# Performance work log

Measured on AMD Instinct MI355X. Metric: run time of the kernel, lower is better.

## Reference

```python
import jax, jax.numpy as jnp
import numpy as np
import math

H = 8        # num_heads
D = 1024     # per-head dim (d_q = d_k = d_v)
D_I = 1024   # image embed dim
D_L = 768    # sentence embed dim
EPS = 1e-5   # nn.LayerNorm default


def setup_inputs() -> dict:
    key = jax.random.key(0)
    ks = jax.random.split(key, 8)
    B, NQ, NK = 8, 196, 128
    img_embed = jax.random.normal(ks[0], (B, NQ, D_I), dtype=jnp.float32)
    sent_embed = jax.random.normal(ks[1], (B, NK, D_L), dtype=jnp.float32)
    atten_mask = jnp.ones((B, NK), dtype=jnp.int32)
    # weights stored [in, out] (equivalent to torch Linear weight.T), no bias
    Wq = jax.random.normal(ks[2], (D_I, H * D), dtype=jnp.float32) * (1.0 / math.sqrt(D_I))
    Wk = jax.random.normal(ks[3], (D_L, H * D), dtype=jnp.float32) * (1.0 / math.sqrt(D_L))
    Wv = jax.random.normal(ks[4], (D_L, H * D), dtype=jnp.float32) * (1.0 / math.sqrt(D_L))
    Wo = jax.random.normal(ks[5], (H * D, D_I), dtype=jnp.float32) * (1.0 / math.sqrt(H * D))
    gamma = jnp.ones((D_I,), dtype=jnp.float32)
    beta = jnp.zeros((D_I,), dtype=jnp.float32)
    return {"img_embed": img_embed, "sent_embed": sent_embed, "atten_mask": atten_mask,
            "Wq": Wq, "Wk": Wk, "Wv": Wv, "Wo": Wo, "gamma": gamma, "beta": beta}


def reference(img_embed, sent_embed, atten_mask, Wq, Wk, Wv, Wo, gamma, beta):
    B = img_embed.shape[0]
    # projections -> [B, N, H, D] -> [B, H, N, D]
    Q = (img_embed @ Wq).reshape(B, -1, H, D).transpose(0, 2, 1, 3)
    K = (sent_embed @ Wk).reshape(B, -1, H, D).transpose(0, 2, 1, 3)
    V = (sent_embed @ Wv).reshape(B, -1, H, D).transpose(0, 2, 1, 3)
    # scaled dot-product scores [B, H, NQ, NK]
    score = jnp.einsum('bhqd,bhkd->bhqk', Q, K) / math.sqrt(D)
    mask = (atten_mask != 0)[:, None, None, :]  # [B,1,1,NK]
    score = jnp.where(mask, score, -jnp.inf)
    attn = jax.nn.softmax(score, axis=-1)
    # PV -> [B, NQ, H, D] -> [B, NQ, H*D]
    ctx = jnp.einsum('bhqk,bhkd->bqhd', attn, V).reshape(B, -1, H * D)
    out = ctx @ Wo + img_embed  # residual
    # LayerNorm over last dim
    mu = jnp.mean(out, axis=-1, keepdims=True)
    var = jnp.var(out, axis=-1, keepdims=True)
    return (out - mu) * jax.lax.rsqrt(var + EPS) * gamma + beta
```

## Files before the change

kernel.cpp:

```cpp
#include <hip/hip_runtime.h>
#include <hip/hip_bf16.h>

#define BB 8
#define NQ 196
#define NKK 128
#define HH 8
#define DH 1024
#define DI 1024
#define DL 768
#define HD 8192
#define KSPLIT 8
#define MTOT (BB * NQ)
#define CHK (MTOT * DH)
#define KVCHK (1024 * 1024)

typedef __attribute__((ext_vector_type(8))) short short8;
typedef __attribute__((ext_vector_type(4))) float f32x4;

__device__ inline unsigned short f2bf(float f) {
  unsigned int x = __float_as_uint(f);
  unsigned int r = (x + 0x7fffu + ((x >> 16) & 1u)) >> 16;
  return (unsigned short)r;
}

__device__ inline void gload16(const unsigned short* g, unsigned short* l) {
  __builtin_amdgcn_global_load_lds(
      (const __attribute__((address_space(1))) void*)g,
      (__attribute__((address_space(3))) void*)l, 16, 0, 0);
}

__device__ __attribute__((always_inline)) inline unsigned ldsOff(const unsigned short* p) {
  return (unsigned)(unsigned long long)
      (__attribute__((address_space(3))) const unsigned short*)p;
}

__device__ __attribute__((always_inline)) inline void gload16a(
    const unsigned short* g, unsigned m0off) {
  unsigned s = __builtin_amdgcn_readfirstlane(m0off);
  asm volatile("s_mov_b32 m0, %1\n\t"
               "global_load_lds_dwordx4 %0, off"
               :: "v"(g), "s"(s) : "m0");
}

__global__ __launch_bounds__(256) void k_prep(
    const float* __restrict__ Wq, const float* __restrict__ Wk,
    const float* __restrict__ Wv, const float* __restrict__ Wo,
    const float* __restrict__ img, const float* __restrict__ sent,
    unsigned short* __restrict__ WqT, unsigned short* __restrict__ WkvT,
    unsigned short* __restrict__ WoT,
    unsigned short* __restrict__ imgB, unsigned short* __restrict__ sentB) {
  int b = blockIdx.x, t = threadIdx.x;
  if (b >= 7168) {
    const float* in; unsigned short* out; int i;
    if (b < 7952) { in = img;  out = imgB;  i = ((b - 7168) * 256 + t) * 8; }
    else          { in = sent; out = sentB; i = ((b - 7952) * 256 + t) * 8; }
    float4 x = *reinterpret_cast<const float4*>(in + i);
    float4 y = *reinterpret_cast<const float4*>(in + i + 4);
    short8 v;
    v[0] = (short)f2bf(x.x); v[1] = (short)f2bf(x.y);
    v[2] = (short)f2bf(x.z); v[3] = (short)f2bf(x.w);
    v[4] = (short)f2bf(y.x); v[5] = (short)f2bf(y.y);
    v[6] = (short)f2bf(y.z); v[7] = (short)f2bf(y.w);
    *reinterpret_cast<short8*>(out + i) = v;
    return;
  }
  const float* in; unsigned short* out; int R, C, bx; bool kcb = false;
  if (b < 2048)      { in = Wq; out = WqT;  R = DI; C = HD; bx = b; }
  else if (b < 3584) { in = Wk; out = WkvT; R = DL; C = HD; bx = b - 2048; }
  else if (b < 5120) { in = Wv; out = WkvT + (size_t)HD * DL; R = DL; C = HD; bx = b - 3584; }
  else               { in = Wo; out = WoT;  R = HD; C = DI; bx = b - 5120; kcb = true; }
  int nxc = C >> 6;
  int c0 = (bx % nxc) << 6, r0 = (bx / nxc) << 6;
  __shared__ float tile[64][65];
#pragma unroll
  for (int p = 0; p < 4; ++p) {
    int row = p * 16 + (t >> 4), c4 = (t & 15) << 2;
    float4 v = *reinterpret_cast<const float4*>(&in[(size_t)(r0 + row) * C + c0 + c4]);
    tile[row][c4] = v.x; tile[row][c4 + 1] = v.y;
    tile[row][c4 + 2] = v.z; tile[row][c4 + 3] = v.w;
  }
  __syncthreads();
#pragma unroll
  for (int p = 0; p < 2; ++p) {
    int cc = p * 32 + (t >> 3), r8 = (t & 7) << 3;
    short8 w;
#pragma unroll
    for (int j = 0; j < 8; ++j) w[j] = (short)f2bf(tile[r8 + j][cc]);
    size_t off;
    if (kcb)
      off = ((size_t)(r0 >> 10) << 20) + (size_t)(c0 + cc) * 1024 + (r0 & 1023) + r8;
    else
      off = (size_t)(c0 + cc) * R + r0 + r8;
    *reinterpret_cast<short8*>(&out[off]) = w;
  }
}

__global__ __launch_bounds__(256) void k_transpose_v(
    const unsigned short* __restrict__ Vbase, unsigned short* __restrict__ Vt) {
  __shared__ unsigned short tile[32][34];
  int z = blockIdx.z, b = z >> 3, h = z & 7;
  const unsigned short* in = Vbase + ((size_t)h << 20) + (size_t)b * NKK * 1024;
  unsigned short* out = Vt + (size_t)z * DH * NKK;
  int d0 = blockIdx.x * 32, k0 = blockIdx.y * 32;
  {
    int rr = threadIdx.x >> 3, c4 = (threadIdx.x & 7) << 2;
    ushort4 v = *reinterpret_cast<const ushort4*>(&in[(size_t)(k0 + rr) * 1024 + d0 + c4]);
    tile[rr][c4] = v.x; tile[rr][c4 + 1] = v.y;
    tile[rr][c4 + 2] = v.z; tile[rr][c4 + 3] = v.w;
  }
  __syncthreads();
  {
    int cc = threadIdx.x >> 3, r4 = (threadIdx.x & 7) << 2;
    ushort4 w;
    w.x = tile[r4][cc];     w.y = tile[r4 + 1][cc];
    w.z = tile[r4 + 2][cc]; w.w = tile[r4 + 3][cc];
    *reinterpret_cast<ushort4*>(&out[(size_t)(d0 + cc) * NKK + k0 + r4]) = w;
  }
}


__device__ __attribute__((always_inline)) inline void ph_pre() {
  __builtin_amdgcn_s_barrier();
  asm volatile("s_waitcnt lgkmcnt(0)" ::: "memory");
  __builtin_amdgcn_sched_barrier(0);
  __builtin_amdgcn_s_setprio(1);
}
__device__ __attribute__((always_inline)) inline void ph_post() {
  __builtin_amdgcn_s_setprio(0);
  __builtin_amdgcn_s_barrier();
}
__device__ __attribute__((always_inline)) inline void ph_post_vm4() {
  __builtin_amdgcn_s_setprio(0);
  asm volatile("s_waitcnt vmcnt(4)" ::: "memory");
  __builtin_amdgcn_s_barrier();
}
__device__ __attribute__((always_inline)) inline void ph_post_vm0() {
  __builtin_amdgcn_s_setprio(0);
  asm volatile("s_waitcnt vmcnt(0)" ::: "memory");
  __builtin_amdgcn_s_barrier();
}

#define LDA8(d, buf, s)                                                          \
  { _Pragma("unroll") for (int mi = 0; mi < 4; ++mi) {                           \
      const int row_ = wm * 128 + (s) * 64 + mi * 16 + fr;                       \
      d[mi][0] = *reinterpret_cast<const short8*>(&As[buf][row_ * 64 + swz0]);   \
      d[mi][1] = *reinterpret_cast<const short8*>(&As[buf][row_ * 64 + swz1]);   \
    } }
#define LDB8(d, buf, s)                                                          \
  { _Pragma("unroll") for (int ni = 0; ni < 2; ++ni) {                           \
      const int row_ = wn * 64 + (s) * 32 + ni * 16 + fr;                        \
      d[ni][0] = *reinterpret_cast<const short8*>(&Bs[buf][row_ * 64 + swz0]);   \
      d[ni][1] = *reinterpret_cast<const short8*>(&Bs[buf][row_ * 64 + swz1]);   \
    } }
#define MMQ(a, sa, b, sb)                                                        \
  { _Pragma("unroll") for (int kk = 0; kk < 2; ++kk) {                           \
      _Pragma("unroll") for (int mi = 0; mi < 4; ++mi) {                         \
        _Pragma("unroll") for (int ni = 0; ni < 2; ++ni)                         \
          acc[(sa) * 4 + mi][(sb) * 2 + ni] =                                    \
              __builtin_amdgcn_mfma_f32_16x16x32_bf16(                           \
                  a[mi][kk], b[ni][kk], acc[(sa) * 4 + mi][(sb) * 2 + ni], 0, 0, 0); \
      } } }
#define STA8(buf, h, kof)                                                        \
  { gload16a(aS[h][0] + (kof), aL + (buf) * 32768 + (h) * 16384);                \
    gload16a(aS[h][1] + (kof), aL + (buf) * 32768 + (h) * 16384 + 8192); }
#define STB8(buf, h, kof)                                                        \
  { gload16a(bS[h][0] + (kof), bL + (buf) * 32768 + (h) * 16384);                \
    gload16a(bS[h][1] + (kof), bL + (buf) * 32768 + (h) * 16384 + 8192); }

struct GCfg {
  const unsigned short* A; const unsigned short* B; void* C;
  int M, K, lda, ldb, ldc, nx, ny;
  long aKC, bKC, cKC;
};

template<bool C_BF16, bool HB>
__global__ __launch_bounds__(512, 2) void k_gemm8(GCfg c0, GCfg c1, int split) {
  __shared__ unsigned short As[2][16384];
  __shared__ unsigned short Bs[2][16384];

  const int seg = (int)blockIdx.x >= split;
  const GCfg cfg = seg ? c1 : c0;
  const int o = (int)blockIdx.x - (seg ? split : 0);
  const int nseg = seg ? ((int)gridDim.x - split) : split;
  const int qq = nseg >> 3;
  const int g = (o & 7) * qq + (o >> 3);
  const int ybl = g % cfg.ny; int t1 = g / cfg.ny;
  const int xbl = t1 % cfg.nx; const int kc = t1 / cfg.nx;

  const int M = cfg.M, lda = cfg.lda, ldb = cfg.ldb;
  const unsigned short* Ab = cfg.A + (size_t)kc * cfg.aKC;
  const unsigned short* Bb = cfg.B + (size_t)kc * cfg.bKC;

  const int tid = threadIdx.x, lane = tid & 63, wid = tid >> 6;
  const int wm = wid >> 2, wn = wid & 3;
  const int m_base = ybl * 256, n_base = xbl * 256;
  const int fr = lane & 15, qk = lane >> 4;
  const int swz0 = ((qk ^ (fr & 7)) << 3);
  const int swz1 = (((4 + qk) ^ (fr & 7)) << 3);

  const int srow = lane >> 3;
  const int sc8 = (((lane & 7) ^ srow) << 3);
  const unsigned short* aS[2][2];
  const unsigned short* bS[2][2];
#pragma unroll
  for (int h = 0; h < 2; ++h)
#pragma unroll
    for (int j = 0; j < 2; ++j) {
      int rm = m_base + h * 128 + j * 64 + wid * 8 + srow;
      rm = rm < M ? rm : M - 1;
      aS[h][j] = Ab + (size_t)rm * lda + sc8;
      bS[h][j] = Bb + (size_t)(n_base + h * 128 + j * 64 + wid * 8 + srow) * ldb + sc8;
    }
  const unsigned aL = ldsOff(&As[0][0]) + (unsigned)(wid * 1024);
  const unsigned bL = ldsOff(&Bs[0][0]) + (unsigned)(wid * 1024);

  short8 a0[4][2], a1[4][2], b0[2][2], b1[2][2];
  f32x4 acc[8][4] = {};

  const int NT = cfg.K >> 6;
  const int NIT = NT >> 1;

  STB8(0, 0, 0) STB8(0, 1, 0) STA8(0, 0, 0) STA8(0, 1, 0)
  STB8(1, 0, 64) STB8(1, 1, 64)
  asm volatile("s_waitcnt vmcnt(4)" ::: "memory");
  __builtin_amdgcn_s_barrier();

  for (int it = 0; it < NIT - 1; ++it) {
    const int t1k = (2 * it + 1) << 6;
    const int t2k = (2 * it + 2) << 6;
    const int t3k = (2 * it + 3) << 6;
    LDA8(a0, 0, 0) LDB8(b0, 0, 0) STA8(1, 0, t1k)
    ph_pre(); MMQ(a0, 0, b0, 0) ph_post();
    LDB8(b1, 0, 1) STA8(1, 1, t1k)
    ph_pre(); MMQ(a0, 0, b1, 1) ph_post();
    LDA8(a1, 0, 1) STB8(0, 0, t2k)
    ph_pre(); MMQ(a1, 1, b1, 1) ph_post();
    STB8(0, 1, t2k)
    ph_pre(); MMQ(a1, 1, b0, 0) ph_post_vm4();
    LDA8(a0, 1, 0) LDB8(b0, 1, 0) STA8(0, 0, t2k)
    ph_pre(); MMQ(a0, 0, b0, 0) ph_post();
    LDB8(b1, 1, 1) STA8(0, 1, t2k)
    ph_pre(); MMQ(a0, 0, b1, 1) ph_post();
    LDA8(a1, 1, 1) STB8(1, 0, t3k)
    ph_pre(); MMQ(a1, 1, b1, 1) ph_post();
    STB8(1, 1, t3k)
    ph_pre(); MMQ(a1, 1, b0, 0) ph_post_vm4();
  }

  {
    const int tlk = (NT - 1) << 6;
    LDA8(a0, 0, 0) LDB8(b0, 0, 0) STA8(1, 0, tlk)
    ph_pre(); MMQ(a0, 0, b0, 0) ph_post();
    LDB8(b1, 0, 1) STA8(1, 1, tlk)
    ph_pre(); MMQ(a0, 0, b1, 1) ph_post();
    LDA8(a1, 0, 1)
    ph_pre(); MMQ(a1, 1, b1, 1) ph_post();
    ph_pre(); MMQ(a1, 1, b0, 0) ph_post_vm0();
    LDA8(a0, 1, 0) LDB8(b0, 1, 0)
    ph_pre(); MMQ(a0, 0, b0, 0) ph_post();
    LDB8(b1, 1, 1)
    ph_pre(); MMQ(a0, 0, b1, 1) ph_post();
    LDA8(a1, 1, 1)
    ph_pre(); MMQ(a1, 1, b1, 1) ph_post();
    ph_pre(); MMQ(a1, 1, b0, 0)
    __builtin_amdgcn_s_setprio(0);
  }

  const size_t cOff = (size_t)kc * cfg.cKC;
  const int ldc = cfg.ldc;
  const int rq4 = qk * 4;
#pragma unroll
  for (int mi = 0; mi < 8; ++mi) {
#pragma unroll
    for (int ni = 0; ni < 4; ++ni) {
      int col = n_base + wn * 64 + ni * 16 + fr;
#pragma unroll
      for (int i = 0; i < 4; ++i) {
        int row = m_base + wm * 128 + mi * 16 + rq4 + i;
        if (row < M) {
          float val = acc[mi][ni][i];
          size_t off;
          if constexpr (HB)
            off = (size_t)(col >> 10) * cfg.cKC + (size_t)row * ldc + (col & 1023);
          else
            off = cOff + (size_t)row * ldc + col;
          if constexpr (C_BF16) ((unsigned short*)cfg.C)[off] = f2bf(val);
          else                  ((float*)cfg.C)[off] = val;
        }
      }
    }
  }
}

template<bool C_BF16>
__global__ __launch_bounds__(256, 2) void k_gemm3(
    const unsigned short* __restrict__ A, const unsigned short* __restrict__ B,
    void* __restrict__ Cptr,
    int M, int K, int lda, int ldb, int ldc,
    int nx, int ny, int ZBH,
    long aSB, long aSH, long bSB, long bSH, long cSB, long cSH,
    long aKC, long bKC, long cKC) {
  __shared__ unsigned short As[8192];
  __shared__ unsigned short Bs[8192];

  const int nblk = gridDim.x;
  const int qq = nblk >> 3, rr = nblk & 7;
  int g;
  { const int o = blockIdx.x, xcd = o & 7, i = o >> 3;
    g = (xcd < rr ? xcd * (qq + 1) : rr * (qq + 1) + (xcd - rr) * qq) + i; }
  const int ybl = g % ny; int t1 = g / ny;
  const int xbl = t1 % nx; const int zz = t1 / nx;
  const int kc = zz / ZBH, bh = zz % ZBH;
  const int zb = bh >> 3, zh = bh & 7;

  const unsigned short* Ab = A + (size_t)zb * aSB + (size_t)zh * aSH + (size_t)kc * aKC;
  const unsigned short* Bb = B + (size_t)zb * bSB + (size_t)zh * bSH + (size_t)kc * bKC;

  const int tid = threadIdx.x, lane = tid & 63, wid = tid >> 6;
  const int wm = wid >> 1, wn = wid & 1;
  const int m_base = ybl * 128, n_base = xbl * 128;

  const int r0 = wid * 32 + (lane >> 3);
  const int sc8 = (((lane & 7) ^ (lane >> 3)) << 3);
  const unsigned short* aSrc[4];
  const unsigned short* bSrc[4];
#pragma unroll
  for (int p = 0; p < 4; ++p) {
    int rm = m_base + r0 + p * 8; rm = rm < M ? rm : M - 1;
    aSrc[p] = Ab + (size_t)rm * lda + sc8;
    bSrc[p] = Bb + (size_t)(n_base + r0 + p * 8) * ldb + sc8;
  }

  const int fr = lane & 15;
  const int qk = lane >> 4;
  f32x4 acc[4][4] = {};

  for (int k0 = 0; k0 < K; k0 += 64) {
#pragma unroll
    for (int p = 0; p < 4; ++p) gload16(aSrc[p] + k0, &As[wid * 2048 + p * 512]);
#pragma unroll
    for (int p = 0; p < 4; ++p) gload16(bSrc[p] + k0, &Bs[wid * 2048 + p * 512]);
    __syncthreads();
#pragma unroll
    for (int kk = 0; kk < 2; ++kk) {
      short8 af[4], bfr[4];
#pragma unroll
      for (int mi = 0; mi < 4; ++mi) {
        int row = wm * 64 + mi * 16 + fr;
        int swz = ((kk * 4 + qk) ^ (row & 7)) << 3;
        af[mi] = *reinterpret_cast<const short8*>(&As[row * 64 + swz]);
      }
#pragma unroll
      for (int ni = 0; ni < 4; ++ni) {
        int row = wn * 64 + ni * 16 + fr;
        int swz = ((kk * 4 + qk) ^ (row & 7)) << 3;
        bfr[ni] = *reinterpret_cast<const short8*>(&Bs[row * 64 + swz]);
      }
#pragma unroll
      for (int mi = 0; mi < 4; ++mi)
#pragma unroll
        for (int ni = 0; ni < 4; ++ni)
          acc[mi][ni] = __builtin_amdgcn_mfma_f32_16x16x32_bf16(af[mi], bfr[ni], acc[mi][ni], 0, 0, 0);
    }
    __syncthreads();
  }

  const size_t cOff = (size_t)zb * cSB + (size_t)zh * cSH + (size_t)kc * cKC;
  const int rq = qk * 4;
#pragma unroll
  for (int mi = 0; mi < 4; ++mi) {
#pragma unroll
    for (int ni = 0; ni < 4; ++ni) {
      int col = n_base + wn * 64 + ni * 16 + fr;
#pragma unroll
      for (int i = 0; i < 4; ++i) {
        int row = m_base + wm * 64 + mi * 16 + rq + i;
        if (row < M) {
          float val = acc[mi][ni][i];
          size_t off = cOff + (size_t)row * ldc + col;
          if constexpr (C_BF16) ((unsigned short*)Cptr)[off] = f2bf(val);
          else                  ((float*)Cptr)[off] = val;
        }
      }
    }
  }
}

#define S_PART ((size_t)64 * NQ * NKK)
__global__ __launch_bounds__(256) void k_softmax(
    const float* __restrict__ S, unsigned short* __restrict__ P, const int* __restrict__ mask) {
  int row = blockIdx.x * 4 + (threadIdx.x >> 6);
  if (row >= BB * HH * NQ) return;
  int lane = threadIdx.x & 63;
  int b = row / (HH * NQ);
  const float* s = S + (size_t)row * NKK;
  float s0 = (s[lane]      + s[lane + S_PART])      * 0.03125f;
  float s1 = (s[lane + 64] + s[lane + 64 + S_PART]) * 0.03125f;
  const int* mrow = mask + b * NKK;
  if (mrow[lane] == 0)      s0 = -1e30f;
  if (mrow[lane + 64] == 0) s1 = -1e30f;
  float mx = fmaxf(s0, s1);
#pragma unroll
  for (int d = 32; d; d >>= 1) mx = fmaxf(mx, __shfl_xor(mx, d));
  float e0 = __expf(s0 - mx), e1 = __expf(s1 - mx);
  float sum = e0 + e1;
#pragma unroll
  for (int d = 32; d; d >>= 1) sum += __shfl_xor(sum, d);
  float inv = 1.0f / sum;
  P[(size_t)row * NKK + lane]      = f2bf(e0 * inv);
  P[(size_t)row * NKK + lane + 64] = f2bf(e1 * inv);
}

__global__ __launch_bounds__(256) void k_layernorm_red(
    const unsigned short* __restrict__ Parts, const float* __restrict__ resid,
    const float* __restrict__ gamma, const float* __restrict__ beta,
    float* __restrict__ out, int M) {
  int row = blockIdx.x;
  int tid = threadIdx.x;
  const size_t stride = (size_t)M * DI;
  const unsigned short* p = Parts + (size_t)row * DI;
  const float* r = resid + (size_t)row * DI;
  float v[4], sum = 0.f, sq = 0.f;
#pragma unroll
  for (int i = 0; i < 4; ++i) {
    int c = tid + i * 256;
    float acc = r[c];
#pragma unroll
    for (int k = 0; k < KSPLIT; ++k)
      acc += __uint_as_float((unsigned)p[k * stride + c] << 16);
    v[i] = acc; sum += acc; sq += acc * acc;
  }
#pragma unroll
  for (int d = 32; d; d >>= 1) { sum += __shfl_xor(sum, d); sq += __shfl_xor(sq, d); }
  __shared__ float ssum[4], ssq[4];
  int w = tid >> 6;
  if ((tid & 63) == 0) { ssum[w] = sum; ssq[w] = sq; }
  __syncthreads();
  sum = ssum[0] + ssum[1] + ssum[2] + ssum[3];
  sq  = ssq[0]  + ssq[1]  + ssq[2]  + ssq[3];
  float mean = sum * (1.0f / DI);
  float var  = sq * (1.0f / DI) - mean * mean;
  float rstd = rsqrtf(var + 1e-5f);
  float* o = out + (size_t)row * DI;
#pragma unroll
  for (int i = 0; i < 4; ++i) {
    int c = tid + i * 256;
    o[c] = (v[i] - mean) * rstd * gamma[c] + beta[c];
  }
}

extern "C" void kernel_launch(void* const* d_in, const int* in_sizes, int n_in,
                              void* d_out, int out_size, void* d_ws, size_t ws_size,
                              hipStream_t stream) {
  const float* img   = (const float*)d_in[0];
  const float* sent  = (const float*)d_in[1];
  const int*   mask  = (const int*)d_in[2];
  const float* Wq    = (const float*)d_in[3];
  const float* Wk    = (const float*)d_in[4];
  const float* Wv    = (const float*)d_in[5];
  const float* Wo    = (const float*)d_in[6];
  const float* gamma = (const float*)d_in[7];
  const float* beta  = (const float*)d_in[8];
  float* out = (float*)d_out;

  char* ws = (char*)d_ws;
  unsigned short* WoT   = (unsigned short*)(ws);
  unsigned short* WkvT  = (unsigned short*)(ws + 16777216);
  unsigned short* Vt    = (unsigned short*)(ws + 16777216);
  unsigned short* Oac   = (unsigned short*)(ws + 16777216);
  float*          S2    = (float*)         (ws + 33554432);
  unsigned short* P     = (unsigned short*)(ws + 46399488);
  unsigned short* Qb    = (unsigned short*)(ws + 49610752);
  unsigned short* KVb   = (unsigned short*)(ws + 75300864);
  unsigned short* ctx   = (unsigned short*)(ws + 75300864);
  unsigned short* WqT   = (unsigned short*)(ws + 75300864);
  unsigned short* imgB  = (unsigned short*)(ws + 92078080);
  unsigned short* sentB = (unsigned short*)(ws + 108855296);

  dim3 tb(256);
  dim3 tb8(512);

  k_prep<<<dim3(8336), tb, 0, stream>>>(Wq, Wk, Wv, Wo, img, sent,
                                        WqT, WkvT, WoT, imgB, sentB);

  GCfg cfgQ  = { imgB,  WqT,  Qb,  MTOT,     DI, DI, DI, 1024, 32, 7, 0, 0, (long)CHK };
  GCfg cfgKV = { sentB, WkvT, KVb, BB * NKK, DL, DL, DL, 1024, 64, 4, 0, 0, (long)KVCHK };
  k_gemm8<true, true><<<dim3(224 + 256), tb8, 0, stream>>>(cfgQ, cfgKV, 224);

  k_transpose_v<<<dim3(DH / 32, NKK / 32, BB * HH), tb, 0, stream>>>(
      KVb + ((size_t)8 << 20), Vt);

  k_gemm3<false><<<dim3(2 * 1 * 128), tb, 0, stream>>>(
      Qb, KVb, S2, NQ, DH / 2, 1024, 1024, NKK,
      1, 2, 64,
      (long)NQ * 1024, (long)CHK,
      (long)NKK * 1024, (long)KVCHK,
      (long)HH * NQ * NKK, (long)NQ * NKK,
      (long)(DH / 2), (long)(DH / 2), (long)64 * NQ * NKK);

  k_softmax<<<dim3(BB * HH * NQ / 4), tb, 0, stream>>>(S2, P, mask);

  k_gemm3<true><<<dim3(2 * 8 * 64), tb, 0, stream>>>(
      P, Vt, ctx, NQ, NKK, NKK, NKK, 1024,
      8, 2, 64,
      (long)HH * NQ * NKK, (long)NQ * NKK,
      (long)HH * DH * NKK, (long)DH * NKK,
      (long)NQ * 1024, (long)CHK,
      0, 0, 0);

  GCfg cfgO = { ctx, WoT, Oac, MTOT, HD / KSPLIT, 1024, 1024, DI, 4, 7,
                (long)CHK, (long)KVCHK, (long)CHK };
  k_gemm8<true, false><<<dim3(224), tb8, 0, stream>>>(cfgO, cfgO, 224);

  k_layernorm_red<<<dim3(BB * NQ), tb, 0, stream>>>(Oac, img, gamma, beta, out, BB * NQ);
}
```

Before: 177.8 us.

## Merge V transpose into softmax launch and run PV with large-tile GEMM

The standalone V-transpose kernel is folded into the softmax kernel as extra blocks (k_mid), which removes one launch and lets the two independent jobs overlap. The P·V product moves from the small k_gemm3 kernel to the 512-thread k_gemm8 kernel. A new PVF epilogue maps each (batch, head) K-chunk index to the ctx layout, and the grid is 256 blocks covering 4 column tiles by 1 row tile per (b,h). The larger 256-row tile covers only 196 valid rows, so some MFMA work is wasted on padding. Mixing two block types in one grid may also unbalance the schedule.

```diff
diff --git a/kernel.cpp b/kernel.cpp
--- a/kernel.cpp
+++ b/kernel.cpp
@@ -92,29 +92,6 @@
     else
       off = (size_t)(c0 + cc) * R + r0 + r8;
     *reinterpret_cast<short8*>(&out[off]) = w;
-  }
-}
-
-__global__ __launch_bounds__(256) void k_transpose_v(
-    const unsigned short* __restrict__ Vbase, unsigned short* __restrict__ Vt) {
-  __shared__ unsigned short tile[32][34];
-  int z = blockIdx.z, b = z >> 3, h = z & 7;
-  const unsigned short* in = Vbase + ((size_t)h << 20) + (size_t)b * NKK * 1024;
-  unsigned short* out = Vt + (size_t)z * DH * NKK;
-  int d0 = blockIdx.x * 32, k0 = blockIdx.y * 32;
-  {
-    int rr = threadIdx.x >> 3, c4 = (threadIdx.x & 7) << 2;
-    ushort4 v = *reinterpret_cast<const ushort4*>(&in[(size_t)(k0 + rr) * 1024 + d0 + c4]);
-    tile[rr][c4] = v.x; tile[rr][c4 + 1] = v.y;
-    tile[rr][c4 + 2] = v.z; tile[rr][c4 + 3] = v.w;
-  }
-  __syncthreads();
-  {
-    int cc = threadIdx.x >> 3, r4 = (threadIdx.x & 7) << 2;
-    ushort4 w;
-    w.x = tile[r4][cc];     w.y = tile[r4 + 1][cc];
-    w.z = tile[r4 + 2][cc]; w.w = tile[r4 + 3][cc];
-    *reinterpret_cast<ushort4*>(&out[(size_t)(d0 + cc) * NKK + k0 + r4]) = w;
   }
 }
 
@@ -173,7 +150,7 @@
   long aKC, bKC, cKC;
 };
 
-template<bool C_BF16, bool HB>
+template<bool C_BF16, bool HB, bool PVF>
 __global__ __launch_bounds__(512, 2) void k_gemm8(GCfg c0, GCfg c1, int split) {
   __shared__ unsigned short As[2][16384];
   __shared__ unsigned short Bs[2][16384];
@@ -280,7 +257,10 @@
         if (row < M) {
           float val = acc[mi][ni][i];
           size_t off;
-          if constexpr (HB)
+          if constexpr (PVF)
+            off = (size_t)(kc & 7) * cfg.cKC
+                + ((size_t)(kc >> 3) * NQ + row) * 1024 + col;
+          else if constexpr (HB)
             off = (size_t)(col >> 10) * cfg.cKC + (size_t)row * ldc + (col & 1023);
           else
             off = cOff + (size_t)row * ldc + col;
@@ -387,9 +367,34 @@
 }
 
 #define S_PART ((size_t)64 * NQ * NKK)
-__global__ __launch_bounds__(256) void k_softmax(
-    const float* __restrict__ S, unsigned short* __restrict__ P, const int* __restrict__ mask) {
-  int row = blockIdx.x * 4 + (threadIdx.x >> 6);
+__global__ __launch_bounds__(256) void k_mid(
+    const unsigned short* __restrict__ Vbase, unsigned short* __restrict__ Vt,
+    const float* __restrict__ S, unsigned short* __restrict__ P,
+    const int* __restrict__ mask) {
+  __shared__ unsigned short tile[32][34];
+  int blk = blockIdx.x;
+  if (blk < 8192) {
+    int z = blk >> 7, b = z >> 3, h = z & 7;
+    int d0 = (blk & 31) * 32, k0 = ((blk >> 5) & 3) * 32;
+    const unsigned short* in = Vbase + ((size_t)h << 20) + (size_t)b * NKK * 1024;
+    unsigned short* out = Vt + (size_t)z * DH * NKK;
+    {
+      int rr = threadIdx.x >> 3, c4 = (threadIdx.x & 7) << 2;
+      ushort4 v = *reinterpret_cast<const ushort4*>(&in[(size_t)(k0 + rr) * 1024 + d0 + c4]);
+      tile[rr][c4] = v.x; tile[rr][c4 + 1] = v.y;
+      tile[rr][c4 + 2] = v.z; tile[rr][c4 + 3] = v.w;
+    }
+    __syncthreads();
+    {
+      int cc = threadIdx.x >> 3, r4 = (threadIdx.x & 7) << 2;
+      ushort4 w;
+      w.x = tile[r4][cc];     w.y = tile[r4 + 1][cc];
+      w.z = tile[r4 + 2][cc]; w.w = tile[r4 + 3][cc];
+      *reinterpret_cast<ushort4*>(&out[(size_t)(d0 + cc) * NKK + k0 + r4]) = w;
+    }
+    return;
+  }
+  int row = (blk - 8192) * 4 + (threadIdx.x >> 6);
   if (row >= BB * HH * NQ) return;
   int lane = threadIdx.x & 63;
   int b = row / (HH * NQ);
@@ -485,10 +490,7 @@
 
   GCfg cfgQ  = { imgB,  WqT,  Qb,  MTOT,     DI, DI, DI, 1024, 32, 7, 0, 0, (long)CHK };
   GCfg cfgKV = { sentB, WkvT, KVb, BB * NKK, DL, DL, DL, 1024, 64, 4, 0, 0, (long)KVCHK };
-  k_gemm8<true, true><<<dim3(224 + 256), tb8, 0, stream>>>(cfgQ, cfgKV, 224);
-
-  k_transpose_v<<<dim3(DH / 32, NKK / 32, BB * HH), tb, 0, stream>>>(
-      KVb + ((size_t)8 << 20), Vt);
+  k_gemm8<true, true, false><<<dim3(224 + 256), tb8, 0, stream>>>(cfgQ, cfgKV, 224);
 
   k_gemm3<false><<<dim3(2 * 1 * 128), tb, 0, stream>>>(
       Qb, KVb, S2, NQ, DH / 2, 1024, 1024, NKK,
@@ -498,19 +500,16 @@
       (long)HH * NQ * NKK, (long)NQ * NKK,
       (long)(DH / 2), (long)(DH / 2), (long)64 * NQ * NKK);
 
-  k_softmax<<<dim3(BB * HH * NQ / 4), tb, 0, stream>>>(S2, P, mask);
-
-  k_gemm3<true><<<dim3(2 * 8 * 64), tb, 0, stream>>>(
-      P, Vt, ctx, NQ, NKK, NKK, NKK, 1024,
-      8, 2, 64,
-      (long)HH * NQ * NKK, (long)NQ * NKK,
-      (long)HH * DH * NKK, (long)DH * NKK,
-      (long)NQ * 1024, (long)CHK,
-      0, 0, 0);
+  k_mid<<<dim3(8192 + (BB * HH * NQ) / 4), tb, 0, stream>>>(
+      KVb + ((size_t)8 << 20), Vt, S2, P, mask);
+
+  GCfg cfgPV = { P, Vt, ctx, NQ, NKK, NKK, NKK, 1024, 4, 1,
+                 (long)NQ * NKK, (long)DH * NKK, (long)CHK };
+  k_gemm8<true, false, true><<<dim3(256), tb8, 0, stream>>>(cfgPV, cfgPV, 256);
 
   GCfg cfgO = { ctx, WoT, Oac, MTOT, HD / KSPLIT, 1024, 1024, DI, 4, 7,
                 (long)CHK, (long)KVCHK, (long)CHK };
-  k_gemm8<true, false><<<dim3(224), tb8, 0, stream>>>(cfgO, cfgO, 224);
+  k_gemm8<true, false, false><<<dim3(224), tb8, 0, stream>>>(cfgO, cfgO, 224);
 
   k_layernorm_red<<<dim3(BB * NQ), tb, 0, stream>>>(Oac, img, gamma, beta, out, BB * NQ);
 }
```

Result: faster. 168.1 us (median of 2 runs) (-5.5%).
